# Kernel tuning notes

Hardware: AMD Instinct MI355X
Metric: run time of the kernel (lower is better)

The kernel has to match this reference:

```python
import jax, jax.numpy as jnp
import numpy as np

B, NLAT, NLON, V = 2, 181, 360, 78
NGRID = NLAT * NLON
NMESH, NEDGE = 10242, 163840
NODE_D, EDGE_D, HID, NLAYERS = 256, 64, 512, 16


def _mlp(x, w1, b1, w2, b2):
    # 2-layer MLP with ReLU (matches MLP(input_dim, hidden_dim, output_dim, n_layers=2))
    return jax.nn.relu(x @ w1 + b1) @ w2 + b2


def setup_inputs() -> dict:
    key = jax.random.key(0)
    ks = jax.random.split(key, 40)
    s = 0.02
    p = {}
    p["x_current"] = jax.random.normal(ks[0], (B, NLAT, NLON, V), jnp.float32)
    p["x_previous"] = jax.random.normal(ks[1], (B, NLAT, NLON, V), jnp.float32)
    p["mesh_node_feats"] = jax.random.normal(ks[2], (NMESH, 7), jnp.float32)
    p["raw_edge_feats"] = jax.random.normal(ks[3], (NEDGE, 4), jnp.float32)
    p["edge_index"] = jax.random.randint(ks[4], (2, NEDGE), 0, NMESH, jnp.int32)
    p["g2m_idx"] = jax.random.randint(ks[5], (NMESH,), 0, NGRID, jnp.int32)  # nearest grid point per mesh node
    p["m2g_idx"] = jax.random.randint(ks[6], (NGRID,), 0, NMESH, jnp.int32)  # nearest mesh node per grid point
    enc_in = 2 * V + 7  # grid channels (current||previous) + 7 mesh geometric features
    p["enc_w1"] = s * jax.random.normal(ks[7], (enc_in, HID), jnp.float32)
    p["enc_b1"] = jnp.zeros((HID,), jnp.float32)
    p["enc_w2"] = s * jax.random.normal(ks[8], (HID, NODE_D), jnp.float32)
    p["enc_b2"] = jnp.zeros((NODE_D,), jnp.float32)
    p["eme_w1"] = s * jax.random.normal(ks[9], (4, EDGE_D), jnp.float32)  # edge_embed: [dx,dy,dz,dist]->edge_dim
    p["eme_b1"] = jnp.zeros((EDGE_D,), jnp.float32)
    p["eme_w2"] = s * jax.random.normal(ks[10], (EDGE_D, EDGE_D), jnp.float32)
    p["eme_b2"] = jnp.zeros((EDGE_D,), jnp.float32)
    e_in = EDGE_D + 2 * NODE_D  # [edge, x_src, x_dst]
    n_in = NODE_D + EDGE_D      # [node, aggregated messages]
    p["pe_w1"] = s * jax.random.normal(ks[11], (NLAYERS, e_in, HID), jnp.float32)
    p["pe_b1"] = jnp.zeros((NLAYERS, HID), jnp.float32)
    p["pe_w2"] = s * jax.random.normal(ks[12], (NLAYERS, HID, EDGE_D), jnp.float32)
    p["pe_b2"] = jnp.zeros((NLAYERS, EDGE_D), jnp.float32)
    p["pn_w1"] = s * jax.random.normal(ks[13], (NLAYERS, n_in, HID), jnp.float32)
    p["pn_b1"] = jnp.zeros((NLAYERS, HID), jnp.float32)
    p["pn_w2"] = s * jax.random.normal(ks[14], (NLAYERS, HID, NODE_D), jnp.float32)
    p["pn_b2"] = jnp.zeros((NLAYERS, NODE_D), jnp.float32)
    p["dec_w1"] = s * jax.random.normal(ks[15], (NODE_D, HID), jnp.float32)
    p["dec_b1"] = jnp.zeros((HID,), jnp.float32)
    p["dec_w2"] = s * jax.random.normal(ks[16], (HID, V), jnp.float32)
    p["dec_b2"] = jnp.zeros((V,), jnp.float32)
    return p


def _forward(x_current, x_previous, mesh_node_feats, raw_edge_feats,
             enc_w1, enc_b1, enc_w2, enc_b2,
             eme_w1, eme_b1, eme_w2, eme_b2,
             pe_w1, pe_b1, pe_w2, pe_b2,
             pn_w1, pn_b1, pn_w2, pn_b2,
             dec_w1, dec_b1, dec_w2, dec_b2,
             edge_index, g2m_idx, m2g_idx):
    # --- Grid -> Mesh encoder ---
    x_input = jnp.concatenate([x_current, x_previous], axis=-1)           # (B, lat, lon, 2V)
    grid_flat = x_input.reshape(B, NGRID, 2 * V)
    gathered = grid_flat[:, g2m_idx]                                      # (B, NMESH, 2V)
    mesh_geo = jnp.broadcast_to(mesh_node_feats[None], (B, NMESH, 7))
    nodes = _mlp(jnp.concatenate([gathered, mesh_geo], -1),
                 enc_w1, enc_b1, enc_w2, enc_b2)                          # (B, NMESH, node_dim)

    # --- Edge embedding (shared initial edges) ---
    edges0 = _mlp(raw_edge_feats, eme_w1, eme_b1, eme_w2, eme_b2)         # (NEDGE, edge_dim)
    src, dst = edge_index[0], edge_index[1]

    def gnn_single(x):
        def layer(carry, params):
            x, e = carry
            w1e, b1e, w2e, b2e, w1n, b1n, w2n, b2n = params
            msg_in = jnp.concatenate([e, x[src], x[dst]], axis=-1)        # (NEDGE, edge+2*node)
            e = e + _mlp(msg_in, w1e, b1e, w2e, b2e)                      # residual edge update
            agg = jax.ops.segment_sum(e, dst, num_segments=NMESH)         # scatter-add to receivers
            x = x + _mlp(jnp.concatenate([x, agg], -1), w1n, b1n, w2n, b2n)
            return (x, e), None
        (x, _), _ = jax.lax.scan(layer, (x, edges0),
                                 (pe_w1, pe_b1, pe_w2, pe_b2, pn_w1, pn_b1, pn_w2, pn_b2))
        return x

    nodes = jax.vmap(gnn_single)(nodes)                                   # batch loop -> vmap

    # --- Mesh -> Grid decoder ---
    grid_nodes = nodes[:, m2g_idx]                                        # (B, NGRID, node_dim)
    delta = _mlp(grid_nodes, dec_w1, dec_b1, dec_w2, dec_b2)              # (B, NGRID, V)
    return delta.reshape(B, NLAT, NLON, V)


def reference(x_current, x_previous, mesh_node_feats, raw_edge_feats,
              enc_w1, enc_b1, enc_w2, enc_b2,
              eme_w1, eme_b1, eme_w2, eme_b2,
              pe_w1, pe_b1, pe_w2, pe_b2,
              pn_w1, pn_b1, pn_w2, pn_b2,
              dec_w1, dec_b1, dec_w2, dec_b2,
              edge_index, g2m_idx, m2g_idx):
    return _forward(x_current, x_previous, mesh_node_feats, raw_edge_feats,
                    enc_w1, enc_b1, enc_w2, enc_b2,
                    eme_w1, eme_b1, eme_w2, eme_b2,
                    pe_w1, pe_b1, pe_w2, pe_b2,
                    pn_w1, pn_b1, pn_w2, pn_b2,
                    dec_w1, dec_b1, dec_w2, dec_b2,
                    edge_index, g2m_idx, m2g_idx)
```

## Files before the change

kernel.cpp:

```cpp
#include <hip/hip_runtime.h>

#define P_NLAT  181
#define P_NLON  360
#define P_V     78
#define P_NGRID (P_NLAT * P_NLON)
#define P_B     2
#define P_NMESH 10242
#define P_NEDGE 163840
#define P_ND    256
#define P_ED    64
#define P_HID   512
#define P_NLAYERS 16

typedef __bf16 bf16x8 __attribute__((ext_vector_type(8)));
typedef unsigned short u16x8 __attribute__((ext_vector_type(8)));
typedef float f32x4 __attribute__((ext_vector_type(4)));

__device__ __forceinline__ unsigned short f2bf(float f) {
  union { float f; unsigned u; } x; x.f = f;
  unsigned r = x.u + 0x7FFFu + ((x.u >> 16) & 1u);
  return (unsigned short)(r >> 16);
}
__device__ __forceinline__ float bf2f(unsigned short h) {
  union { unsigned u; float f; } x; x.u = ((unsigned)h) << 16; return x.f;
}

__device__ __forceinline__ void gl_lds16(const unsigned short* gp, unsigned short* lp) {
  __builtin_amdgcn_global_load_lds(
      (const __attribute__((address_space(1))) unsigned int*)gp,
      (__attribute__((address_space(3))) unsigned int*)lp, 16, 0, 0);
}

struct GArgs {
  int amode;
  const unsigned short* A; long lda; long a_bstride;
  const int* gidx; int gr_off; int gr_per_b; int gsrc_rows_per_b;
  int M, K;
  const unsigned short* Wt;
  const float* bias; int Nreal; int relu;
  unsigned short* out16; long ldo16; long o16_bstride; long dup16;
  float* out32; long ldo32; long o32_bstride; long dup32;
  const float* resid; long r_bstride;
};

#define BM 128

template<int BN, int WM, int WN>
__global__ void __launch_bounds__(256) gemm_k(GArgs g) {
  constexpr int MI = WM / 16, NJ = WN / 16;
  constexpr int WPN = BN / WN;
  __shared__ unsigned short As[BM * 64];
  __shared__ unsigned short Bs[BN * 64];

  const int tid  = threadIdx.x;
  const int lane = tid & 63, wid = tid >> 6;
  const int wm = (wid / WPN) * WM, wn = (wid % WPN) * WN;
  const int bm = blockIdx.x * BM;
  const int bn = blockIdx.y * BN;
  const int z  = blockIdx.z;

  const unsigned short* Ad = g.A + (long)z * g.a_bstride;

  f32x4 acc[MI][NJ];
  #pragma unroll
  for (int i = 0; i < MI; ++i)
    #pragma unroll
    for (int j = 0; j < NJ; ++j) { f32x4 zv = {0.f, 0.f, 0.f, 0.f}; acc[i][j] = zv; }

  const int nKt = g.K >> 6;
  for (int kt = 0; kt < nKt; ++kt) {
    const int k0 = kt << 6;
    #pragma unroll
    for (int it = 0; it < (BM * 8) / 256; ++it) {
      int v = tid + it * 256;
      int r = v >> 3, j = v & 7;
      int row = bm + r; if (row >= g.M) row = g.M - 1;
      int kk = k0 + ((j ^ (r & 7)) << 3);
      const unsigned short* s;
      if (g.amode == 0) {
        s = Ad + (long)row * g.lda + kk;
      } else {
        int gr = g.gr_off + row;
        int b = gr / g.gr_per_b, loc = gr - b * g.gr_per_b;
        s = g.A + ((long)b * g.gsrc_rows_per_b + g.gidx[loc]) * g.lda + kk;
      }
      gl_lds16(s, &As[v << 3]);
    }
    #pragma unroll
    for (int it = 0; it < (BN * 8) / 256; ++it) {
      int v = tid + it * 256;
      int n = v >> 3, j = v & 7;
      gl_lds16(g.Wt + (long)(bn + n) * g.K + k0 + ((j ^ (n & 7)) << 3), &Bs[v << 3]);
    }
    __syncthreads();
    #pragma unroll
    for (int ko = 0; ko < 2; ++ko) {
      bf16x8 af[MI], bfr[NJ];
      #pragma unroll
      for (int i = 0; i < MI; ++i) {
        int ar = wm + i * 16 + (lane & 15);
        int ch = ((ko * 4 + (lane >> 4)) ^ (ar & 7)) << 3;
        u16x8 t = *(const u16x8*)&As[ar * 64 + ch];
        af[i] = __builtin_bit_cast(bf16x8, t);
      }
      #pragma unroll
      for (int j = 0; j < NJ; ++j) {
        int br = wn + j * 16 + (lane & 15);
        int ch = ((ko * 4 + (lane >> 4)) ^ (br & 7)) << 3;
        u16x8 t = *(const u16x8*)&Bs[br * 64 + ch];
        bfr[j] = __builtin_bit_cast(bf16x8, t);
      }
      #pragma unroll
      for (int i = 0; i < MI; ++i)
        #pragma unroll
        for (int j = 0; j < NJ; ++j)
          acc[i][j] = __builtin_amdgcn_mfma_f32_16x16x32_bf16(af[i], bfr[j], acc[i][j], 0, 0, 0);
    }
    __syncthreads();
  }

  unsigned short* o16 = g.out16 ? g.out16 + (long)z * g.o16_bstride : (unsigned short*)0;
  float* o32 = g.out32 ? g.out32 + (long)z * g.o32_bstride : (float*)0;
  const float* res = g.resid ? g.resid + (long)z * g.r_bstride : (const float*)0;
  const int q = lane >> 4, cc = lane & 15;
  #pragma unroll
  for (int i = 0; i < MI; ++i) {
    #pragma unroll
    for (int r = 0; r < 4; ++r) {
      int row = bm + wm + i * 16 + q * 4 + r;
      if (row >= g.M) continue;
      const float* rr = res ? res + (long)row * g.ldo32 : (const float*)0;
      #pragma unroll
      for (int j = 0; j < NJ; ++j) {
        int col = bn + wn + j * 16 + cc;
        if (col >= g.Nreal) continue;
        float v = acc[i][j][r];
        if (g.bias) v += g.bias[col];
        if (rr) v += rr[col];
        if (g.relu && v < 0.f) v = 0.f;
        if (o32) {
          long idx = (long)row * g.ldo32 + col;
          o32[idx] = v; if (g.dup32) o32[idx + g.dup32] = v;
        }
        if (o16) {
          long idx = (long)row * g.ldo16 + col;
          unsigned short h = f2bf(v);
          o16[idx] = h; if (g.dup16) o16[idx + g.dup16] = h;
        }
      }
    }
  }
}

struct FEArgs {
  unsigned short* E16;
  float* E32;
  const unsigned short* PSPD;
  const int* srcP; const int* dstP;
  const unsigned short* W1t;
  const unsigned short* W2t;
  const float* b1; const float* b2;
};

__global__ void __launch_bounds__(256) fused_edge(FEArgs g) {
  __shared__ unsigned short As[64 * 64];
  __shared__ float Hs32[64 * 132];
  __shared__ unsigned short U1[64 * 136];
  __shared__ unsigned short B2s[64 * 128];

  const int tid = threadIdx.x, lane = tid & 63, wid = tid >> 6;
  const int q = lane >> 4, cc = lane & 15;
  const int z = blockIdx.y;
  const long gr0 = (long)blockIdx.x * 64;
  const long EB = (long)P_NEDGE * 64;
  unsigned short* E16z = g.E16 + z * EB;
  float* E32z = g.E32 + z * EB;
  const int moff = z * P_NMESH;

  #pragma unroll
  for (int it = 0; it < 2; ++it) {
    int v = tid + it * 256;
    int r = v >> 3, j = v & 7;
    gl_lds16(E16z + (gr0 + r) * 64 + ((j ^ (r & 7)) << 3), &As[v << 3]);
  }

  const int wm1 = (wid >> 1) * 32, wn1 = (wid & 1) * 64;
  const int wm2 = wid * 16;

  f32x4 acc2[4];
  #pragma unroll
  for (int j = 0; j < 4; ++j) { f32x4 zv = {0.f, 0.f, 0.f, 0.f}; acc2[j] = zv; }

  for (int hc = 0; hc < 4; ++hc) {
    #pragma unroll
    for (int it = 0; it < 4; ++it) {
      int v = tid + it * 256;
      int n = v >> 3, j = v & 7;
      gl_lds16(g.W1t + (long)(hc * 128 + n) * 64 + ((j ^ (n & 7)) << 3), &U1[v << 3]);
    }
    __syncthreads();

    f32x4 acc1[2][4];
    #pragma unroll
    for (int i = 0; i < 2; ++i)
      #pragma unroll
      for (int j = 0; j < 4; ++j) { f32x4 zv = {0.f, 0.f, 0.f, 0.f}; acc1[i][j] = zv; }
    #pragma unroll
    for (int ko = 0; ko < 2; ++ko) {
      bf16x8 af[2], bfr[4];
      #pragma unroll
      for (int i = 0; i < 2; ++i) {
        int ar = wm1 + i * 16 + cc;
        int ch = ((ko * 4 + q) ^ (ar & 7)) << 3;
        u16x8 t = *(const u16x8*)&As[ar * 64 + ch];
        af[i] = __builtin_bit_cast(bf16x8, t);
      }
      #pragma unroll
      for (int j = 0; j < 4; ++j) {
        int n = wn1 + j * 16 + cc;
        int ch = ((ko * 4 + q) ^ (n & 7)) << 3;
        u16x8 t = *(const u16x8*)&U1[n * 64 + ch];
        bfr[j] = __builtin_bit_cast(bf16x8, t);
      }
      #pragma unroll
      for (int i = 0; i < 2; ++i)
        #pragma unroll
        for (int j = 0; j < 4; ++j)
          acc1[i][j] = __builtin_amdgcn_mfma_f32_16x16x32_bf16(af[i], bfr[j], acc1[i][j], 0, 0, 0);
    }
    #pragma unroll
    for (int i = 0; i < 2; ++i)
      #pragma unroll
      for (int j = 0; j < 4; ++j)
        #pragma unroll
        for (int r = 0; r < 4; ++r)
          Hs32[(wm1 + i * 16 + q * 4 + r) * 132 + wn1 + j * 16 + cc] = acc1[i][j][r];
    __syncthreads();

    #pragma unroll
    for (int it = 0; it < 4; ++it) {
      int v = tid + it * 256;
      int r = v >> 4, c8 = (v & 15) << 3;
      long grow = gr0 + r;
      const unsigned short* ps = g.PSPD + ((long)(moff + g.srcP[grow])) * 1024 + hc * 128 + c8;
      const unsigned short* pd = g.PSPD + ((long)(moff + g.dstP[grow])) * 1024 + 512 + hc * 128 + c8;
      u16x8 psv = *(const u16x8*)ps;
      u16x8 pdv = *(const u16x8*)pd;
      f32x4 ha = *(const f32x4*)&Hs32[r * 132 + c8];
      f32x4 hb = *(const f32x4*)&Hs32[r * 132 + c8 + 4];
      const float* b1p = g.b1 + hc * 128 + c8;
      u16x8 outv;
      #pragma unroll
      for (int e = 0; e < 8; ++e) {
        float x = (e < 4 ? ha[e] : hb[e - 4]) + b1p[e] + bf2f(psv[e]) + bf2f(pdv[e]);
        outv[e] = f2bf(x < 0.f ? 0.f : x);
      }
      *(u16x8*)&U1[r * 136 + c8] = outv;
    }
    #pragma unroll
    for (int it = 0; it < 4; ++it) {
      int v = tid + it * 256;
      int n = v >> 4, j = v & 15;
      gl_lds16(g.W2t + (long)n * 512 + hc * 128 + ((j ^ (n & 7)) << 3), &B2s[v << 3]);
    }
    __syncthreads();

    #pragma unroll
    for (int ko = 0; ko < 4; ++ko) {
      int ar = wm2 + cc;
      u16x8 ta = *(const u16x8*)&U1[ar * 136 + ko * 32 + q * 8];
      bf16x8 af = __builtin_bit_cast(bf16x8, ta);
      #pragma unroll
      for (int j = 0; j < 4; ++j) {
        int n = j * 16 + cc;
        int ch = ((ko * 4 + q) ^ (n & 7)) << 3;
        u16x8 tb = *(const u16x8*)&B2s[n * 128 + ch];
        bf16x8 bf = __builtin_bit_cast(bf16x8, tb);
        acc2[j] = __builtin_amdgcn_mfma_f32_16x16x32_bf16(af, bf, acc2[j], 0, 0, 0);
      }
    }
    __syncthreads();
  }

  #pragma unroll
  for (int j = 0; j < 4; ++j) {
    #pragma unroll
    for (int r = 0; r < 4; ++r) {
      int row = wm2 + q * 4 + r;
      int col = j * 16 + cc;
      long idx = (gr0 + row) * 64 + col;
      float v = acc2[j][r] + g.b2[col] + E32z[idx];
      E32z[idx] = v;
      E16z[idx] = f2bf(v);
    }
  }
}

__global__ void wt_conv(const float* W, unsigned short* Wt, int K, int N, int Kpad, int Npad,
                        int row_off, long in_lstride, long out_lstride) {
  long t = (long)blockIdx.x * 256 + threadIdx.x;
  long tot = (long)Npad * Kpad;
  if (t >= tot) return;
  int n = (int)(t / Kpad), k = (int)(t - (long)n * Kpad);
  const float* Wl = W + (long)blockIdx.z * in_lstride + (long)row_off * N;
  float v = (n < N && k < K) ? Wl[(long)k * N + n] : 0.f;
  Wt[(long)blockIdx.z * out_lstride + t] = f2bf(v);
}

__global__ void build_enc_in(const float* xc, const float* xp, const float* mesh,
                             const int* g2m, unsigned short* out) {
  long t = (long)blockIdx.x * 256 + threadIdx.x;
  const long tot = (long)P_B * P_NMESH * 192;
  if (t >= tot) return;
  int k = (int)(t % 192); long r = t / 192;
  int m = (int)(r % P_NMESH); int b = (int)(r / P_NMESH);
  float v = 0.f;
  if (k < P_V)              v = xc[((long)b * P_NGRID + g2m[m]) * P_V + k];
  else if (k < 2 * P_V)     v = xp[((long)b * P_NGRID + g2m[m]) * P_V + (k - P_V)];
  else if (k < 2 * P_V + 7) v = mesh[m * 7 + (k - 2 * P_V)];
  out[t] = f2bf(v);
}

__global__ void build_rawpad(const float* raw, const int* perm, unsigned short* out) {
  long t = (long)blockIdx.x * 256 + threadIdx.x;
  const long tot = (long)P_NEDGE * 64;
  if (t >= tot) return;
  int k = (int)(t & 63); long r = t >> 6;
  int e = perm[r];
  out[t] = f2bf(k < 4 ? raw[(long)e * 4 + k] : 0.f);
}

__global__ void csr_hist(const int* dst, int* cnt) {
  int e = blockIdx.x * 256 + threadIdx.x;
  if (e < P_NEDGE) atomicAdd(&cnt[dst[e]], 1);
}
__global__ void csr_scan(const int* cnt, int* rowptr) {
  __shared__ int part[1024];
  int t = threadIdx.x;
  const int C = (P_NMESH + 1023) / 1024;
  int base = t * C, s = 0;
  for (int i = 0; i < C; ++i) { int idx = base + i; if (idx < P_NMESH) s += cnt[idx]; }
  part[t] = s; __syncthreads();
  for (int ofs = 1; ofs < 1024; ofs <<= 1) {
    int v = (t >= ofs) ? part[t - ofs] : 0;
    __syncthreads();
    part[t] += v;
    __syncthreads();
  }
  int excl = (t == 0) ? 0 : part[t - 1];
  for (int i = 0; i < C; ++i) {
    int idx = base + i;
    if (idx < P_NMESH) { rowptr[idx] = excl; excl += cnt[idx]; }
  }
  if (t == 1023) rowptr[P_NMESH] = excl;
}
__global__ void csr_scatter(const int* dst, const int* rowptr, int* cursor, int* perm) {
  int e = blockIdx.x * 256 + threadIdx.x;
  if (e < P_NEDGE) {
    int d = dst[e];
    int pos = atomicAdd(&cursor[d], 1);
    perm[rowptr[d] + pos] = e;
  }
}
__global__ void csr_permsd(const int* perm, const int* src, const int* dst, int* srcP, int* dstP) {
  int i = blockIdx.x * 256 + threadIdx.x;
  if (i < P_NEDGE) { int p = perm[i]; srcP[i] = src[p]; dstP[i] = dst[p]; }
}

__global__ void seg_reduce(const float* E32, const int* rowptr, unsigned short* XN) {
  int node = blockIdx.x * 4 + (threadIdx.x >> 6);
  int c = threadIdx.x & 63;
  int b = blockIdx.y;
  if (node >= P_NMESH) return;
  int r0 = rowptr[node], r1 = rowptr[node + 1];
  const float* base = E32 + (long)b * P_NEDGE * 64;
  float s = 0.f;
  for (int r = r0; r < r1; ++r) s += base[(long)r * 64 + c];
  XN[((long)b * P_NMESH + node) * 320 + 256 + c] = f2bf(s);
}

extern "C" void kernel_launch(void* const* d_in, const int* in_sizes, int n_in,
                              void* d_out, int out_size, void* d_ws, size_t ws_size,
                              hipStream_t stream) {
  (void)in_sizes; (void)n_in; (void)out_size;
  const float* x_current  = (const float*)d_in[0];
  const float* x_previous = (const float*)d_in[1];
  const float* mesh_feats = (const float*)d_in[2];
  const float* raw_edge   = (const float*)d_in[3];
  const int*   edge_index = (const int*)d_in[4];
  const int*   g2m        = (const int*)d_in[5];
  const int*   m2g        = (const int*)d_in[6];
  const float* enc_w1 = (const float*)d_in[7];
  const float* enc_b1 = (const float*)d_in[8];
  const float* enc_w2 = (const float*)d_in[9];
  const float* enc_b2 = (const float*)d_in[10];
  const float* eme_w1 = (const float*)d_in[11];
  const float* eme_b1 = (const float*)d_in[12];
  const float* eme_w2 = (const float*)d_in[13];
  const float* eme_b2 = (const float*)d_in[14];
  const float* pe_w1 = (const float*)d_in[15];
  const float* pe_b1 = (const float*)d_in[16];
  const float* pe_w2 = (const float*)d_in[17];
  const float* pe_b2 = (const float*)d_in[18];
  const float* pn_w1 = (const float*)d_in[19];
  const float* pn_b1 = (const float*)d_in[20];
  const float* pn_w2 = (const float*)d_in[21];
  const float* pn_b2 = (const float*)d_in[22];
  const float* dec_w1 = (const float*)d_in[23];
  const float* dec_b1 = (const float*)d_in[24];
  const float* dec_w2 = (const float*)d_in[25];
  const float* dec_b2 = (const float*)d_in[26];
  const int* srcI = edge_index;
  const int* dstI = edge_index + P_NEDGE;
  float* out = (float*)d_out;

  char* wsb = (char*)d_ws; size_t off = 0;
  auto alloc = [&](size_t bytes) -> void* {
    off = (off + 255) & ~(size_t)255;
    void* p = wsb + off; off += bytes; return p;
  };
  auto au16 = [&](long n) { return (unsigned short*)alloc((size_t)n * 2); };
  auto af32 = [&](long n) { return (float*)alloc((size_t)n * 4); };
  auto ai32 = [&](long n) { return (int*)alloc((size_t)n * 4); };

  unsigned short* enc_w1t   = au16(512L * 192);
  unsigned short* enc_w2t   = au16(256L * 512);
  unsigned short* eme_w1t   = au16(64L * 64);
  unsigned short* eme_w2t   = au16(64L * 64);
  unsigned short* pe_w1e_t  = au16(16L * 512 * 64);
  unsigned short* pe_w1sd_t = au16(16L * 1024 * 256);
  unsigned short* pe_w2t    = au16(16L * 64 * 512);
  unsigned short* pn_w1t    = au16(16L * 512 * 320);
  unsigned short* pn_w2t    = au16(16L * 256 * 512);
  unsigned short* dec_w1t   = au16(512L * 256);
  unsigned short* dec_w2t   = au16(128L * 512);
  int* cnt    = ai32(P_NMESH);
  int* cursor = ai32(P_NMESH);
  int* rowptr = ai32(P_NMESH + 1);
  int* perm   = ai32(P_NEDGE);
  int* srcP   = ai32(P_NEDGE);
  int* dstP   = ai32(P_NEDGE);
  float*          X32 = af32((long)P_B * P_NMESH * P_ND);
  unsigned short* XN  = au16((long)P_B * P_NMESH * 320);
  float*          E32 = af32((long)P_B * P_NEDGE * P_ED);
  unsigned short* E16 = au16((long)P_B * P_NEDGE * P_ED);
  size_t encin_b  = ((size_t)P_B * P_NMESH * 192 * 2 + 255) & ~(size_t)255;
  size_t rawpad_b = ((size_t)P_NEDGE * 64 * 2 + 255) & ~(size_t)255;
  size_t pspd_b   = ((size_t)P_B * P_NMESH * 1024 * 2 + 255) & ~(size_t)255;
  size_t reg1_b   = encin_b + rawpad_b; if (pspd_b > reg1_b) reg1_b = pspd_b;
  char* region1 = (char*)alloc(reg1_b);
  unsigned short* ENCIN  = (unsigned short*)region1;
  unsigned short* RAWPAD = (unsigned short*)(region1 + encin_b);
  unsigned short* PSPD   = (unsigned short*)region1;

  size_t rem = (ws_size > off + 4096) ? ws_size - off - 4096 : 0;
  size_t hb_full = (size_t)P_B * P_NGRID * 512 * 2;
  int DC; size_t hb;
  if (rem >= hb_full)          { DC = 1; hb = hb_full; }
  else if (rem >= hb_full / 2) { DC = 2; hb = hb_full / 2; }
  else                         { DC = 4; hb = hb_full / 4; }
  unsigned short* HBUF = (unsigned short*)alloc(hb);

  auto run128 = [&](const GArgs& a, int Npad, int zdim) {
    dim3 grid((a.M + BM - 1) / BM, Npad / 128, zdim);
    gemm_k<128, 64, 64><<<grid, dim3(256), 0, stream>>>(a);
  };
  auto run64 = [&](const GArgs& a, int zdim) {
    dim3 grid((a.M + BM - 1) / BM, 1, zdim);
    gemm_k<64, 32, 64><<<grid, dim3(256), 0, stream>>>(a);
  };
  auto convw = [&](const float* W, unsigned short* Wt, int K, int N, int Kp, int Np,
                   int row_off, long in_lst, long out_lst, int L) {
    long tot = (long)Np * Kp;
    wt_conv<<<dim3((unsigned)((tot + 255) / 256), 1, L), dim3(256), 0, stream>>>(
        W, Wt, K, N, Kp, Np, row_off, in_lst, out_lst);
  };

  hipMemsetAsync(cnt, 0, P_NMESH * 4, stream);
  hipMemsetAsync(cursor, 0, P_NMESH * 4, stream);
  csr_hist<<<dim3(P_NEDGE / 256), dim3(256), 0, stream>>>(dstI, cnt);
  csr_scan<<<dim3(1), dim3(1024), 0, stream>>>(cnt, rowptr);
  csr_scatter<<<dim3(P_NEDGE / 256), dim3(256), 0, stream>>>(dstI, rowptr, cursor, perm);
  csr_permsd<<<dim3(P_NEDGE / 256), dim3(256), 0, stream>>>(perm, srcI, dstI, srcP, dstP);

  convw(enc_w1, enc_w1t, 163, 512, 192, 512, 0, 163L * 512, 192L * 512, 1);
  convw(enc_w2, enc_w2t, 512, 256, 512, 256, 0, 512L * 256, 512L * 256, 1);
  convw(eme_w1, eme_w1t, 4, 64, 64, 64, 0, 4L * 64, 64L * 64, 1);
  convw(eme_w2, eme_w2t, 64, 64, 64, 64, 0, 64L * 64, 64L * 64, 1);
  convw(pe_w1, pe_w1e_t, 64, 512, 64, 512, 0, 576L * 512, 512L * 64, 16);
  convw(pe_w1, pe_w1sd_t, 256, 512, 256, 512, 64, 576L * 512, 1024L * 256, 16);
  convw(pe_w1, pe_w1sd_t + 512L * 256, 256, 512, 256, 512, 320, 576L * 512, 1024L * 256, 16);
  convw(pe_w2, pe_w2t, 512, 64, 512, 64, 0, 512L * 64, 64L * 512, 16);
  convw(pn_w1, pn_w1t, 320, 512, 320, 512, 0, 320L * 512, 512L * 320, 16);
  convw(pn_w2, pn_w2t, 512, 256, 512, 256, 0, 512L * 256, 256L * 512, 16);
  convw(dec_w1, dec_w1t, 256, 512, 256, 512, 0, 256L * 512, 512L * 256, 1);
  convw(dec_w2, dec_w2t, 512, 78, 512, 128, 0, 512L * 78, 128L * 512, 1);

  { long tot = (long)P_B * P_NMESH * 192;
    build_enc_in<<<dim3((unsigned)((tot + 255) / 256)), dim3(256), 0, stream>>>(
        x_current, x_previous, mesh_feats, g2m, ENCIN); }
  { long tot = (long)P_NEDGE * 64;
    build_rawpad<<<dim3((unsigned)((tot + 255) / 256)), dim3(256), 0, stream>>>(
        raw_edge, perm, RAWPAD); }

  { GArgs a{}; a.amode = 0; a.A = ENCIN; a.lda = 192; a.M = P_B * P_NMESH; a.K = 192;
    a.Wt = enc_w1t; a.bias = enc_b1; a.Nreal = 512; a.relu = 1;
    a.out16 = HBUF; a.ldo16 = 512; run128(a, 512, 1); }
  { GArgs a{}; a.amode = 0; a.A = HBUF; a.lda = 512; a.M = P_B * P_NMESH; a.K = 512;
    a.Wt = enc_w2t; a.bias = enc_b2; a.Nreal = 256; a.relu = 0;
    a.out32 = X32; a.ldo32 = 256; a.out16 = XN; a.ldo16 = 320; run128(a, 256, 1); }

  { GArgs a{}; a.amode = 0; a.A = RAWPAD; a.lda = 64; a.M = P_NEDGE; a.K = 64;
    a.Wt = eme_w1t; a.bias = eme_b1; a.Nreal = 64; a.relu = 1;
    a.out16 = HBUF; a.ldo16 = 64; run64(a, 1); }
  { GArgs a{}; a.amode = 0; a.A = HBUF; a.lda = 64; a.M = P_NEDGE; a.K = 64;
    a.Wt = eme_w2t; a.bias = eme_b2; a.Nreal = 64; a.relu = 0;
    a.out32 = E32; a.ldo32 = 64; a.dup32 = (long)P_NEDGE * 64;
    a.out16 = E16; a.ldo16 = 64; a.dup16 = (long)P_NEDGE * 64; run64(a, 1); }

  for (int l = 0; l < P_NLAYERS; ++l) {
    { GArgs a{}; a.amode = 0; a.A = XN; a.lda = 320; a.M = P_B * P_NMESH; a.K = 256;
      a.Wt = pe_w1sd_t + (long)l * 1024 * 256; a.Nreal = 1024; a.relu = 0;
      a.out16 = PSPD; a.ldo16 = 1024; run128(a, 1024, 1); }
    { FEArgs f{}; f.E16 = E16; f.E32 = E32; f.PSPD = PSPD;
      f.srcP = srcP; f.dstP = dstP;
      f.W1t = pe_w1e_t + (long)l * 512 * 64;
      f.W2t = pe_w2t + (long)l * 64 * 512;
      f.b1 = pe_b1 + l * 512; f.b2 = pe_b2 + l * 64;
      fused_edge<<<dim3(P_NEDGE / 64, P_B), dim3(256), 0, stream>>>(f); }
    seg_reduce<<<dim3((P_NMESH + 3) / 4, P_B), dim3(256), 0, stream>>>(E32, rowptr, XN);
    { GArgs a{}; a.amode = 0; a.A = XN; a.lda = 320; a.M = P_B * P_NMESH; a.K = 320;
      a.Wt = pn_w1t + (long)l * 512 * 320; a.bias = pn_b1 + l * 512; a.Nreal = 512; a.relu = 1;
      a.out16 = HBUF; a.ldo16 = 512; run128(a, 512, 1); }
    { GArgs a{}; a.amode = 0; a.A = HBUF; a.lda = 512; a.M = P_B * P_NMESH; a.K = 512;
      a.Wt = pn_w2t + (long)l * 256 * 512; a.bias = pn_b2 + l * 256; a.Nreal = 256; a.relu = 0;
      a.resid = X32; a.out32 = X32; a.ldo32 = 256; a.out16 = XN; a.ldo16 = 320;
      run128(a, 256, 1); }
  }

  const int dcrows = (P_B * P_NGRID) / DC;
  for (int c = 0; c < DC; ++c) {
    int c0 = c * dcrows;
    { GArgs a{}; a.amode = 2; a.A = XN; a.lda = 320;
      a.gidx = m2g; a.gr_off = c0; a.gr_per_b = P_NGRID; a.gsrc_rows_per_b = P_NMESH;
      a.M = dcrows; a.K = 256;
      a.Wt = dec_w1t; a.bias = dec_b1; a.Nreal = 512; a.relu = 1;
      a.out16 = HBUF; a.ldo16 = 512; run128(a, 512, 1); }
    { GArgs a{}; a.amode = 0; a.A = HBUF; a.lda = 512; a.M = dcrows; a.K = 512;
      a.Wt = dec_w2t; a.bias = dec_b2; a.Nreal = 78; a.relu = 0;
      a.out32 = out + (long)c0 * P_V; a.ldo32 = P_V;
      run128(a, 128, 1); }
  }
}
```

Baseline: 5.593 ms.

## Shrink fused edge kernel LDS by halving hidden chunk and reusing buffers

The fused edge MLP kernel now walks the 512-wide hidden dimension in eight chunks of 64 instead of four chunks of 128. The hidden tile's fp32 buffer is reused in place as the swizzled bf16 activation buffer, and one weight buffer serves both W1 and W2. LDS per block drops from roughly 66KB to about 34KB, and launch bounds ask for 4 blocks per CU to raise occupancy and hide the gather latency. The cost is twice as many loop iterations and barriers, plus an extra sync, since the activations are held in registers before they overwrite the shared buffer.

```diff
diff --git a/kernel.cpp b/kernel.cpp
--- a/kernel.cpp
+++ b/kernel.cpp
@@ -162,11 +162,10 @@
   const float* b1; const float* b2;
 };
 
-__global__ void __launch_bounds__(256) fused_edge(FEArgs g) {
+__global__ void __launch_bounds__(256, 4) fused_edge(FEArgs g) {
   __shared__ unsigned short As[64 * 64];
-  __shared__ float Hs32[64 * 132];
-  __shared__ unsigned short U1[64 * 136];
-  __shared__ unsigned short B2s[64 * 128];
+  __shared__ float HS[64 * 68];
+  __shared__ unsigned short WS[64 * 64];
 
   const int tid = threadIdx.x, lane = tid & 63, wid = tid >> 6;
   const int q = lane >> 4, cc = lane & 15;
@@ -176,6 +175,8 @@
   unsigned short* E16z = g.E16 + z * EB;
   float* E32z = g.E32 + z * EB;
   const int moff = z * P_NMESH;
+  unsigned short* HSb = (unsigned short*)HS;
+  const int wm = wid * 16;
 
   #pragma unroll
   for (int it = 0; it < 2; ++it) {
@@ -184,97 +185,89 @@
     gl_lds16(E16z + (gr0 + r) * 64 + ((j ^ (r & 7)) << 3), &As[v << 3]);
   }
 
-  const int wm1 = (wid >> 1) * 32, wn1 = (wid & 1) * 64;
-  const int wm2 = wid * 16;
-
   f32x4 acc2[4];
   #pragma unroll
   for (int j = 0; j < 4; ++j) { f32x4 zv = {0.f, 0.f, 0.f, 0.f}; acc2[j] = zv; }
 
-  for (int hc = 0; hc < 4; ++hc) {
-    #pragma unroll
-    for (int it = 0; it < 4; ++it) {
+  for (int hc = 0; hc < 8; ++hc) {
+    #pragma unroll
+    for (int it = 0; it < 2; ++it) {
       int v = tid + it * 256;
       int n = v >> 3, j = v & 7;
-      gl_lds16(g.W1t + (long)(hc * 128 + n) * 64 + ((j ^ (n & 7)) << 3), &U1[v << 3]);
-    }
-    __syncthreads();
-
-    f32x4 acc1[2][4];
-    #pragma unroll
-    for (int i = 0; i < 2; ++i)
-      #pragma unroll
-      for (int j = 0; j < 4; ++j) { f32x4 zv = {0.f, 0.f, 0.f, 0.f}; acc1[i][j] = zv; }
+      gl_lds16(g.W1t + (long)(hc * 64 + n) * 64 + ((j ^ (n & 7)) << 3), &WS[v << 3]);
+    }
+    __syncthreads();
+
+    f32x4 acc1[4];
+    #pragma unroll
+    for (int j = 0; j < 4; ++j) { f32x4 zv = {0.f, 0.f, 0.f, 0.f}; acc1[j] = zv; }
     #pragma unroll
     for (int ko = 0; ko < 2; ++ko) {
-      bf16x8 af[2], bfr[4];
-      #pragma unroll
-      for (int i = 0; i < 2; ++i) {
-        int ar = wm1 + i * 16 + cc;
-        int ch = ((ko * 4 + q) ^ (ar & 7)) << 3;
-        u16x8 t = *(const u16x8*)&As[ar * 64 + ch];
-        af[i] = __builtin_bit_cast(bf16x8, t);
-      }
+      int ar = wm + cc;
+      u16x8 ta = *(const u16x8*)&As[ar * 64 + (((ko * 4 + q) ^ (ar & 7)) << 3)];
+      bf16x8 af = __builtin_bit_cast(bf16x8, ta);
       #pragma unroll
       for (int j = 0; j < 4; ++j) {
-        int n = wn1 + j * 16 + cc;
-        int ch = ((ko * 4 + q) ^ (n & 7)) << 3;
-        u16x8 t = *(const u16x8*)&U1[n * 64 + ch];
-        bfr[j] = __builtin_bit_cast(bf16x8, t);
-      }
-      #pragma unroll
-      for (int i = 0; i < 2; ++i)
-        #pragma unroll
-        for (int j = 0; j < 4; ++j)
-          acc1[i][j] = __builtin_amdgcn_mfma_f32_16x16x32_bf16(af[i], bfr[j], acc1[i][j], 0, 0, 0);
-    }
-    #pragma unroll
-    for (int i = 0; i < 2; ++i)
-      #pragma unroll
-      for (int j = 0; j < 4; ++j)
-        #pragma unroll
-        for (int r = 0; r < 4; ++r)
-          Hs32[(wm1 + i * 16 + q * 4 + r) * 132 + wn1 + j * 16 + cc] = acc1[i][j][r];
-    __syncthreads();
-
-    #pragma unroll
-    for (int it = 0; it < 4; ++it) {
+        int n = j * 16 + cc;
+        u16x8 tb = *(const u16x8*)&WS[n * 64 + (((ko * 4 + q) ^ (n & 7)) << 3)];
+        bf16x8 bf = __builtin_bit_cast(bf16x8, tb);
+        acc1[j] = __builtin_amdgcn_mfma_f32_16x16x32_bf16(af, bf, acc1[j], 0, 0, 0);
+      }
+    }
+    #pragma unroll
+    for (int j = 0; j < 4; ++j)
+      #pragma unroll
+      for (int r = 0; r < 4; ++r)
+        HS[(wm + q * 4 + r) * 68 + j * 16 + cc] = acc1[j][r];
+    __syncthreads();
+
+    #pragma unroll
+    for (int it = 0; it < 2; ++it) {
       int v = tid + it * 256;
-      int r = v >> 4, c8 = (v & 15) << 3;
+      int n = v >> 3, j = v & 7;
+      gl_lds16(g.W2t + (long)n * 512 + hc * 64 + ((j ^ (n & 7)) << 3), &WS[v << 3]);
+    }
+    float hv[2][8];
+    #pragma unroll
+    for (int it = 0; it < 2; ++it) {
+      int v = tid + it * 256;
+      int r = v >> 3, c8 = (v & 7) << 3;
       long grow = gr0 + r;
-      const unsigned short* ps = g.PSPD + ((long)(moff + g.srcP[grow])) * 1024 + hc * 128 + c8;
-      const unsigned short* pd = g.PSPD + ((long)(moff + g.dstP[grow])) * 1024 + 512 + hc * 128 + c8;
+      const unsigned short* ps = g.PSPD + (long)(moff + g.srcP[grow]) * 1024 + hc * 64 + c8;
+      const unsigned short* pd = g.PSPD + (long)(moff + g.dstP[grow]) * 1024 + 512 + hc * 64 + c8;
       u16x8 psv = *(const u16x8*)ps;
       u16x8 pdv = *(const u16x8*)pd;
-      f32x4 ha = *(const f32x4*)&Hs32[r * 132 + c8];
-      f32x4 hb = *(const f32x4*)&Hs32[r * 132 + c8 + 4];
-      const float* b1p = g.b1 + hc * 128 + c8;
-      u16x8 outv;
+      f32x4 ha = *(const f32x4*)&HS[r * 68 + c8];
+      f32x4 hb = *(const f32x4*)&HS[r * 68 + c8 + 4];
+      const float* b1p = g.b1 + hc * 64 + c8;
       #pragma unroll
       for (int e = 0; e < 8; ++e) {
         float x = (e < 4 ? ha[e] : hb[e - 4]) + b1p[e] + bf2f(psv[e]) + bf2f(pdv[e]);
-        outv[e] = f2bf(x < 0.f ? 0.f : x);
-      }
-      *(u16x8*)&U1[r * 136 + c8] = outv;
-    }
-    #pragma unroll
-    for (int it = 0; it < 4; ++it) {
+        hv[it][e] = x < 0.f ? 0.f : x;
+      }
+    }
+    __syncthreads();
+
+    #pragma unroll
+    for (int it = 0; it < 2; ++it) {
       int v = tid + it * 256;
-      int n = v >> 4, j = v & 15;
-      gl_lds16(g.W2t + (long)n * 512 + hc * 128 + ((j ^ (n & 7)) << 3), &B2s[v << 3]);
-    }
-    __syncthreads();
-
-    #pragma unroll
-    for (int ko = 0; ko < 4; ++ko) {
-      int ar = wm2 + cc;
-      u16x8 ta = *(const u16x8*)&U1[ar * 136 + ko * 32 + q * 8];
+      int r = v >> 3, j = v & 7;
+      u16x8 outv;
+      #pragma unroll
+      for (int e = 0; e < 8; ++e) outv[e] = f2bf(hv[it][e]);
+      *(u16x8*)&HSb[r * 64 + ((j ^ (r & 7)) << 3)] = outv;
+    }
+    __syncthreads();
+
+    #pragma unroll
+    for (int ko = 0; ko < 2; ++ko) {
+      int ar = wm + cc;
+      u16x8 ta = *(const u16x8*)&HSb[ar * 64 + (((ko * 4 + q) ^ (ar & 7)) << 3)];
       bf16x8 af = __builtin_bit_cast(bf16x8, ta);
       #pragma unroll
       for (int j = 0; j < 4; ++j) {
         int n = j * 16 + cc;
-        int ch = ((ko * 4 + q) ^ (n & 7)) << 3;
-        u16x8 tb = *(const u16x8*)&B2s[n * 128 + ch];
+        u16x8 tb = *(const u16x8*)&WS[n * 64 + (((ko * 4 + q) ^ (n & 7)) << 3)];
         bf16x8 bf = __builtin_bit_cast(bf16x8, tb);
         acc2[j] = __builtin_amdgcn_mfma_f32_16x16x32_bf16(af, bf, acc2[j], 0, 0, 0);
       }
@@ -286,7 +279,7 @@
   for (int j = 0; j < 4; ++j) {
     #pragma unroll
     for (int r = 0; r < 4; ++r) {
-      int row = wm2 + q * 4 + r;
+      int row = wm + q * 4 + r;
       int col = j * 16 + cc;
       long idx = (gr0 + row) * 64 + col;
       float v = acc2[j][r] + g.b2[col] + E32z[idx];
```

New measurement: 5.015 ms. -10.3%, faster.
